# Optimization experiments

Hardware: AMD Instinct MI355X
Metric: run time of the kernel (lower is better)

Reference implementation:

```python
import jax, jax.numpy as jnp
import numpy as np

B, L, E, F, H, V = 64, 32, 512, 512, 1024, 10000


def setup_inputs() -> dict:
    key = jax.random.key(0)
    ks = jax.random.split(key, 20)
    def lin_w(k, out_d, in_d):
        # 4 stacked gate weights (i, f, o, c), PyTorch Linear-style scale
        s = 1.0 / np.sqrt(in_d)
        return jax.random.uniform(k, (4, out_d, in_d), jnp.float32, -s, s)
    def lin_b(k, out_d, in_d):
        s = 1.0 / np.sqrt(in_d)
        return jax.random.uniform(k, (4, out_d), jnp.float32, -s, s)
    inp = {
        "captions": jax.random.randint(ks[0], (B, L), 0, V),
        "image_features": jax.random.normal(ks[1], (B, E), jnp.float32),
        "B_emb": jax.random.normal(ks[2], (V, E), jnp.float32),
        "V_W": lin_w(ks[3], F, E), "V_b": lin_b(ks[4], F, E),
        "S_W": lin_w(ks[5], F, F), "S_b": lin_b(ks[6], F, F),
        "U_W": lin_w(ks[7], H, F), "U_b": lin_b(ks[8], H, F),
        "W_W": lin_w(ks[9], H, H), "W_b": lin_b(ks[10], H, H),
        "C_W": jax.random.uniform(ks[11], (V, H), jnp.float32, -1.0/np.sqrt(H), 1.0/np.sqrt(H)),
        "C_b": jax.random.uniform(ks[12], (V,), jnp.float32, -1.0/np.sqrt(H), 1.0/np.sqrt(H)),
        # original uses nn.init.uniform_ on fresh tensors -> U[0,1)
        "h0": jax.random.uniform(ks[13], (B, H), jnp.float32),
        "c0": jax.random.uniform(ks[14], (B, H), jnp.float32),
    }
    return inp


def reference(captions, image_features, B_emb, V_W, V_b, S_W, S_b, U_W, U_b,
              W_W, W_b, C_W, C_b, h0, c0):
    emb = B_emb[captions]                                   # [B, L, E]
    embedded = jnp.concatenate([image_features[:, None, :], emb], axis=1)  # [B, L+1, E]
    x = embedded[:, :-1, :]                                 # [B, T, E], T = L
    # input-dependent gate pre-activations (V -> S_d[mode] -> U), independent of h
    g = jnp.einsum('bte,gfe->btgf', x, V_W) + V_b           # [B, T, 4, F]
    g = jnp.einsum('btgf,gof->btgo', g, S_W) + S_b          # [B, T, 4, F]
    g = jnp.einsum('btgf,ghf->btgh', g, U_W) + U_b          # [B, T, 4, H]

    def step(carry, g_t):
        h, c = carry
        hg = jnp.einsum('bk,ghk->bgh', h, W_W) + W_b        # [B, 4, H]
        z = g_t + hg
        i_t = jax.nn.sigmoid(z[:, 0])
        f_t = jax.nn.sigmoid(z[:, 1])
        o_t = jax.nn.sigmoid(z[:, 2])
        c_tilda = jnp.tanh(z[:, 3])
        c_new = f_t * c + i_t * c_tilda
        h_new = o_t * c_new
        logits = h_new @ C_W.T + C_b                        # [B, V]
        return (h_new, c_new), logits

    _, outs = jax.lax.scan(step, (h0, c0), jnp.swapaxes(g, 0, 1))  # outs: [T, B, V]
    return jnp.swapaxes(outs, 0, 1)                         # [B, T, V]
```

## Files before the change

### kernel.cpp

```cpp
#include <hip/hip_runtime.h>
#include <hip/hip_bf16.h>

typedef __attribute__((ext_vector_type(8))) __bf16 bf16x8;
typedef __attribute__((ext_vector_type(4))) float f32x4;
typedef unsigned short ushort_t;

#define Bdim 64
#define Tdim 32
#define Edim 512
#define Fdim 512
#define Hdim 1024
#define Vdim 10000
#define SCAN_BLOCKS 64

__device__ __forceinline__ float bf2f(ushort_t u) {
    unsigned int x = ((unsigned int)u) << 16;
    union { unsigned int i; float f; } c; c.i = x; return c.f;
}
__device__ __forceinline__ ushort_t f2bf(float f) {
    __hip_bfloat16 h = __float2bfloat16(f);
    union { __hip_bfloat16 h; ushort_t u; } c; c.h = h; return c.u;
}

__device__ __forceinline__ void gload_lds16(const void* g, void* l) {
    __builtin_amdgcn_global_load_lds(
        (const __attribute__((address_space(1))) unsigned int*)g,
        (__attribute__((address_space(3))) unsigned int*)l, 16, 0, 0);
}

__device__ __forceinline__ void store_short_wt(ushort_t* p, ushort_t v) {
    asm volatile("global_store_short %0, %1, off sc0 sc1"
                 : : "v"(p), "v"((unsigned int)v) : "memory");
}
__device__ __forceinline__ void store_uint_wt(unsigned int* p, unsigned int v) {
    asm volatile("global_store_dword %0, %1, off sc0 sc1"
                 : : "v"(p), "v"(v) : "memory");
}

__global__ void cvt_all(const float* __restrict__ vw, const float* __restrict__ sw,
                        const float* __restrict__ uw, const float* __restrict__ ww,
                        const float* __restrict__ cw, const float* __restrict__ h0,
                        ushort_t* __restrict__ mir, unsigned int* __restrict__ flg) {
    if (blockIdx.x == 0) {
        int4 zz = {0, 0, 0, 0};
        ((int4*)flg)[threadIdx.x * 2 + 0] = zz;
        ((int4*)flg)[threadIdx.x * 2 + 1] = zz;
    }
    long idx = ((long)blockIdx.x * blockDim.x + threadIdx.x) * 8;
    const float* src; long off;
    if      (idx <  1048576L) { src = vw; off = idx; }
    else if (idx <  2097152L) { src = sw; off = idx - 1048576L; }
    else if (idx <  4194304L) { src = uw; off = idx - 2097152L; }
    else if (idx <  8388608L) { src = ww; off = idx - 4194304L; }
    else if (idx < 18628608L) { src = cw; off = idx - 8388608L; }
    else if (idx < 18694144L) { src = h0; off = idx - 18628608L; }
    else return;
    float4 a = *(const float4*)(src + off);
    float4 b = *(const float4*)(src + off + 4);
    ushort_t o[8];
    o[0] = f2bf(a.x); o[1] = f2bf(a.y); o[2] = f2bf(a.z); o[3] = f2bf(a.w);
    o[4] = f2bf(b.x); o[5] = f2bf(b.y); o[6] = f2bf(b.z); o[7] = f2bf(b.w);
    *(int4*)(mir + idx) = *(const int4*)o;
}

__global__ void build_x(const int* __restrict__ cap,
                        const float* __restrict__ img,
                        const float* __restrict__ emb,
                        ushort_t* __restrict__ X) {
    int idx = blockIdx.x * blockDim.x + threadIdx.x;
    int row = idx >> 6;
    int c8  = (idx & 63) << 3;
    int b = row >> 5, t = row & 31;
    const float* src = (t == 0) ? (img + (size_t)b * Edim)
                                : (emb + (size_t)cap[b * Tdim + (t - 1)] * Edim);
    float4 a  = *(const float4*)(src + c8);
    float4 bb = *(const float4*)(src + c8 + 4);
    ushort_t o[8];
    o[0] = f2bf(a.x);  o[1] = f2bf(a.y);  o[2] = f2bf(a.z);  o[3] = f2bf(a.w);
    o[4] = f2bf(bb.x); o[5] = f2bf(bb.y); o[6] = f2bf(bb.z); o[7] = f2bf(bb.w);
    *(int4*)(X + (size_t)row * Edim + c8) = *(const int4*)o;
}

__launch_bounds__(256)
__global__ void gemm_bt(const ushort_t* __restrict__ A, long lda, long gsA,
                        const ushort_t* __restrict__ Bm, long ldb, long gsB,
                        void* __restrict__ Cv, long ldc, long gsC,
                        const float* __restrict__ bias, long gsBias,
                        int N, int K, int f32out, int zpack, int aswap) {
    __shared__ ushort_t As[128 * 64];
    __shared__ ushort_t Bs[128 * 64];
    int z = blockIdx.z;
    A += (size_t)z * gsA; Bm += (size_t)z * gsB; bias += (size_t)z * gsBias;

    int nx = gridDim.x, ny = gridDim.y;
    int lin = blockIdx.x + nx * blockIdx.y;
    int per_xcd = (nx * ny) >> 3;
    int l2 = (lin & 7) * per_xcd + (lin >> 3);
    int bx = l2 / ny, by = l2 % ny;

    int tid = threadIdx.x;
    int w = tid >> 6, l = tid & 63;
    int wm = (w >> 1) * 64, wn = (w & 1) * 64;
    int m0 = by * 128, n0 = bx * 128;

    int srow = tid >> 3;
    int scol = (tid & 7) << 3;

    int lane_r = l & 15;
    int lane_k = (l >> 4) << 3;

    f32x4 zero = {0.f, 0.f, 0.f, 0.f};
    f32x4 acc[4][4];
#pragma unroll
    for (int i = 0; i < 4; i++)
#pragma unroll
        for (int j = 0; j < 4; j++) acc[i][j] = zero;

    for (int k0 = 0; k0 < K; k0 += 64) {
#pragma unroll
        for (int j = 0; j < 4; j++) {
            int r = srow + j * 32;
            int pr = m0 + r;
            if (aswap) pr = ((pr & 31) << 6) + (pr >> 5);
            int sc = scol ^ ((r & 7) << 3);
            gload_lds16(A + (size_t)pr * lda + k0 + sc, &As[r * 64 + scol]);
        }
#pragma unroll
        for (int j = 0; j < 4; j++) {
            int r = srow + j * 32;
            int br = n0 + r; if (br > N - 1) br = N - 1;
            int sc = scol ^ ((r & 7) << 3);
            gload_lds16(Bm + (size_t)br * ldb + k0 + sc, &Bs[r * 64 + scol]);
        }
        __syncthreads();
#pragma unroll
        for (int kk = 0; kk < 64; kk += 32) {
            bf16x8 af[4], bfr[4];
#pragma unroll
            for (int i = 0; i < 4; i++) {
                int ar = wm + i * 16 + lane_r;
                af[i] = *(const bf16x8*)&As[ar * 64 + ((kk + lane_k) ^ ((ar & 7) << 3))];
            }
#pragma unroll
            for (int j = 0; j < 4; j++) {
                int br2 = wn + j * 16 + lane_r;
                bfr[j] = *(const bf16x8*)&Bs[br2 * 64 + ((kk + lane_k) ^ ((br2 & 7) << 3))];
            }
#pragma unroll
            for (int i = 0; i < 4; i++)
#pragma unroll
                for (int j = 0; j < 4; j++)
                    acc[i][j] = __builtin_amdgcn_mfma_f32_16x16x32_bf16(af[i], bfr[j], acc[i][j], 0, 0, 0);
        }
        __syncthreads();
    }

    int row_base = m0 + wm + ((l >> 4) << 2);
    int col_base = n0 + wn + lane_r;
#pragma unroll
    for (int j = 0; j < 4; j++) {
        int col = col_base + j * 16;
        if (col < N) {
            float bv = bias[col];
#pragma unroll
            for (int i = 0; i < 4; i++) {
#pragma unroll
                for (int r = 0; r < 4; r++) {
                    int row = row_base + i * 16 + r;
                    float v = acc[i][j][r] + bv;
                    if (zpack) {
                        int b = row >> 5, tt = row & 31;
                        size_t idx = (((size_t)(tt * 64 + (col >> 4)) * 4 + z) * 16
                                      + (col & 15)) * 64 + b;
                        ((ushort_t*)Cv)[idx] = f2bf(v);
                    } else if (f32out) {
                        ((float*)Cv)[(size_t)z * gsC + (size_t)row * ldc + col] = v;
                    } else {
                        ((ushort_t*)Cv)[(size_t)z * gsC + (size_t)row * ldc + col] = f2bf(v);
                    }
                }
            }
        }
    }
}

#define GLD(i, o) asm volatile("global_load_dwordx4 %0, %1, off offset:" o \
                               : "=v"(ab[i]) : "v"(apx))
#define CHUNK(d, n, ISSUE)                                                                   \
    do {                                                                                     \
        const int kc2 = ((d) * 32 + lane_kb) * 2;                                            \
        bf16x8 b0 = *(const bf16x8*)((const char*)Ws + ((     lane_r) * 2048 + (kc2 ^ swz)));\
        bf16x8 b1 = *(const bf16x8*)((const char*)Ws + ((16 + lane_r) * 2048 + (kc2 ^ swz)));\
        bf16x8 b2 = *(const bf16x8*)((const char*)Ws + ((32 + lane_r) * 2048 + (kc2 ^ swz)));\
        bf16x8 b3 = *(const bf16x8*)((const char*)Ws + ((48 + lane_r) * 2048 + (kc2 ^ swz)));\
        asm volatile("s_waitcnt vmcnt(" n ")");                                              \
        __builtin_amdgcn_sched_barrier(0);                                                   \
        bf16x8 av = __builtin_bit_cast(bf16x8, ab[(d) & 15]);                                \
        acc[0] = __builtin_amdgcn_mfma_f32_16x16x32_bf16(av, b0, acc[0], 0, 0, 0);           \
        acc[1] = __builtin_amdgcn_mfma_f32_16x16x32_bf16(av, b1, acc[1], 0, 0, 0);           \
        acc[2] = __builtin_amdgcn_mfma_f32_16x16x32_bf16(av, b2, acc[2], 0, 0, 0);           \
        acc[3] = __builtin_amdgcn_mfma_f32_16x16x32_bf16(av, b3, acc[3], 0, 0, 0);           \
        ISSUE;                                                                               \
    } while (0)

__launch_bounds__(256, 1)
__global__ void lstm_scan(const ushort_t* __restrict__ Wm,
                          const float* __restrict__ Wb,
                          const ushort_t* __restrict__ zb,
                          const ushort_t* __restrict__ h0b,
                          const float* __restrict__ c0,
                          ushort_t* __restrict__ Hbt,
                          unsigned int* __restrict__ flags) {
    __shared__ ushort_t Ws[64 * 1024];
    int cg = blockIdx.x;
    int tid = threadIdx.x;
    int w = tid >> 6, l = tid & 63;
    int lane_r = l & 15, lane_kb = (l >> 4) << 3;

    for (int e = tid * 8; e < 65536; e += 2048) {
        int rowl = e >> 10, ke = e & 1023;
        int g = rowl >> 4, hc = rowl & 15;
        const ushort_t* src = Wm + ((size_t)(g * Hdim + cg * 16 + hc)) * Hdim + ke;
        int dstb = rowl * 2048 + ((ke * 2) ^ ((rowl & 7) << 4));
        *(int4*)((char*)Ws + dstb) = *(const int4*)src;
    }
    int hcol = cg * 16 + lane_r;
    float wbv[4];
#pragma unroll
    for (int g = 0; g < 4; g++) wbv[g] = Wb[g * Hdim + hcol];
    int rb0 = w * 16 + ((l >> 4) << 2);
    float cst[4];
#pragma unroll
    for (int r = 0; r < 4; r++) cst[r] = c0[(size_t)(rb0 + r) * Hdim + hcol];
    __syncthreads();

    int arow = w * 16 + lane_r;
    int swz = (lane_r & 7) << 4;

    for (int t = 0; t < Tdim; t++) {
        ushort_t g3s[4][4];
        size_t zbase = ((size_t)t * 64 + cg) * 4096 + (size_t)lane_r * 64 + rb0;
#pragma unroll
        for (int g = 0; g < 4; g++)
            *(ushort4*)g3s[g] = *(const ushort4*)(zb + zbase + (size_t)g * 1024);

        if (t > 0) {
            const unsigned int* fp = flags + (size_t)(t - 1) * 64 + l;
            unsigned int v;
            do {
                v = __hip_atomic_load(fp, __ATOMIC_RELAXED, __HIP_MEMORY_SCOPE_AGENT);
            } while (__ballot(v != 0) != 0xFFFFFFFFFFFFFFFFull);
        }
        __builtin_amdgcn_sched_barrier(0);

        const ushort_t* hp = t ? (Hbt + (size_t)(t - 1) * (Bdim * Hdim)) : h0b;
        const ushort_t* apx = hp + (size_t)arow * Hdim + lane_kb;

        int4 ab[16];
        GLD(0, "0");    GLD(1, "64");   GLD(2, "128");  GLD(3, "192");
        GLD(4, "256");  GLD(5, "320");  GLD(6, "384");  GLD(7, "448");
        GLD(8, "512");  GLD(9, "576");  GLD(10, "640"); GLD(11, "704");
        GLD(12, "768"); GLD(13, "832"); GLD(14, "896"); GLD(15, "960");

        f32x4 zero = {0.f, 0.f, 0.f, 0.f};
        f32x4 acc[4];
#pragma unroll
        for (int g = 0; g < 4; g++) acc[g] = zero;

        CHUNK(0, "15", GLD(0, "1024"));  CHUNK(1, "15", GLD(1, "1088"));
        CHUNK(2, "15", GLD(2, "1152"));  CHUNK(3, "15", GLD(3, "1216"));
        CHUNK(4, "15", GLD(4, "1280"));  CHUNK(5, "15", GLD(5, "1344"));
        CHUNK(6, "15", GLD(6, "1408"));  CHUNK(7, "15", GLD(7, "1472"));
        CHUNK(8, "15", GLD(8, "1536"));  CHUNK(9, "15", GLD(9, "1600"));
        CHUNK(10, "15", GLD(10, "1664")); CHUNK(11, "15", GLD(11, "1728"));
        CHUNK(12, "15", GLD(12, "1792")); CHUNK(13, "15", GLD(13, "1856"));
        CHUNK(14, "15", GLD(14, "1920")); CHUNK(15, "15", GLD(15, "1984"));
        CHUNK(16, "15", (void)0); CHUNK(17, "14", (void)0);
        CHUNK(18, "13", (void)0); CHUNK(19, "12", (void)0);
        CHUNK(20, "11", (void)0); CHUNK(21, "10", (void)0);
        CHUNK(22, "9", (void)0);  CHUNK(23, "8", (void)0);
        CHUNK(24, "7", (void)0);  CHUNK(25, "6", (void)0);
        CHUNK(26, "5", (void)0);  CHUNK(27, "4", (void)0);
        CHUNK(28, "3", (void)0);  CHUNK(29, "2", (void)0);
        CHUNK(30, "1", (void)0);  CHUNK(31, "0", (void)0);

#pragma unroll
        for (int r = 0; r < 4; r++) {
            float zi = acc[0][r] + wbv[0] + bf2f(g3s[0][r]);
            float zf = acc[1][r] + wbv[1] + bf2f(g3s[1][r]);
            float zo = acc[2][r] + wbv[2] + bf2f(g3s[2][r]);
            float zc = acc[3][r] + wbv[3] + bf2f(g3s[3][r]);
            float it = __builtin_amdgcn_rcpf(1.f + __expf(-zi));
            float ft = __builtin_amdgcn_rcpf(1.f + __expf(-zf));
            float ot = __builtin_amdgcn_rcpf(1.f + __expf(-zo));
            float e2 = __expf(-2.f * zc);
            float ct = (1.f - e2) * __builtin_amdgcn_rcpf(1.f + e2);
            float cn = ft * cst[r] + it * ct;
            cst[r] = cn;
            store_short_wt(Hbt + (size_t)t * (Bdim * Hdim) + (size_t)(rb0 + r) * Hdim + hcol,
                           f2bf(ot * cn));
        }

        asm volatile("s_waitcnt vmcnt(0)" ::: "memory");
        __syncthreads();
        if (tid == 0) store_uint_wt(flags + (size_t)t * 64 + cg, 1u);
    }
}

extern "C" void kernel_launch(void* const* d_in, const int* in_sizes, int n_in,
                              void* d_out, int out_size, void* d_ws, size_t ws_size,
                              hipStream_t stream) {
    const int*   cap  = (const int*)d_in[0];
    const float* img  = (const float*)d_in[1];
    const float* Bemb = (const float*)d_in[2];
    const float* V_W  = (const float*)d_in[3];
    const float* V_b  = (const float*)d_in[4];
    const float* S_W  = (const float*)d_in[5];
    const float* S_b  = (const float*)d_in[6];
    const float* U_W  = (const float*)d_in[7];
    const float* U_b  = (const float*)d_in[8];
    const float* W_W  = (const float*)d_in[9];
    const float* W_b  = (const float*)d_in[10];
    const float* C_W  = (const float*)d_in[11];
    const float* C_b  = (const float*)d_in[12];
    const float* h0   = (const float*)d_in[13];
    const float* c0   = (const float*)d_in[14];

    char* ws = (char*)d_ws;
    ushort_t* mir = (ushort_t*)(ws);
    ushort_t* X   = (ushort_t*)(ws + (size_t)(36u << 20));
    ushort_t* g1  = (ushort_t*)(ws + (size_t)(38u << 20));
    ushort_t* g2  = (ushort_t*)(ws + (size_t)(46u << 20));
    ushort_t* Hbt = (ushort_t*)(ws + (size_t)(54u << 20));
    unsigned int* flags = (unsigned int*)(ws + (size_t)(58u << 20));
    ushort_t* zb  = (ushort_t*)d_out;

    const ushort_t* V_Wb = mir;
    const ushort_t* S_Wb = mir + 1048576L;
    const ushort_t* U_Wb = mir + 2097152L;
    const ushort_t* W_Wb = mir + 4194304L;
    const ushort_t* C_Wb = mir + 8388608L;
    const ushort_t* h0b  = mir + 18628608L;

    cvt_all<<<9128, 256, 0, stream>>>(V_W, S_W, U_W, W_W, C_W, h0, mir, flags);
    build_x<<<512, 256, 0, stream>>>(cap, img, Bemb, X);

    gemm_bt<<<dim3(16, 16, 1), 256, 0, stream>>>(X, 512, 0, V_Wb, 512, 0,
                                                 g1, 2048, 0, V_b, 0, 2048, 512, 0, 0, 0);
    gemm_bt<<<dim3(4, 16, 4), 256, 0, stream>>>(g1, 2048, 512, S_Wb, 512, 512 * 512,
                                                g2, 2048, 512, S_b, 512, 512, 512, 0, 0, 0);
    gemm_bt<<<dim3(8, 16, 4), 256, 0, stream>>>(g2, 2048, 512, U_Wb, 512, 1024 * 512,
                                                zb, 0, 0, U_b, 1024, 1024, 512, 0, 1, 0);
    {
        const ushort_t* a0 = W_Wb; const float* a1 = W_b; const ushort_t* a2 = zb;
        const ushort_t* a3 = h0b;  const float* a4 = c0;  ushort_t* a5 = Hbt;
        unsigned int* a6 = flags;
        void* sargs[7] = {(void*)&a0, (void*)&a1, (void*)&a2, (void*)&a3,
                          (void*)&a4, (void*)&a5, (void*)&a6};
        hipLaunchCooperativeKernel((const void*)lstm_scan, dim3(SCAN_BLOCKS), dim3(256),
                                   sargs, 0, stream);
    }
    gemm_bt<<<dim3(79, 16, 1), 256, 0, stream>>>(Hbt, 1024, 0, C_Wb, 1024, 0,
                                                 d_out, 10000, 0, C_b, 0,
                                                 10000, 1024, 1, 0, 1);
}
```

Measured before the change: 384.1 us.

## Split LSTM scan across 256 blocks with per-block 4-column gate slices

The recurrent scan now runs on 256 workgroups, each owning 4 hidden columns (16 gate rows) instead of 16 columns, so the per-step W_h matmul work per block drops fourfold and more CUs share the latency-bound loop. Gate pre-activations are packed in a new layout, one MFMA tile covers all four gates, and lane shuffles regroup i/f/o/c per column. Completion flags become bytes polled four at a time as dwords, and the B-operand LDS read is software-pipelined one chunk ahead. The cost is more blocks to synchronise per timestep and redundant h loads across blocks.

Result: slower. 545.4 us (+42.0%).

```diff
diff --git a/kernel.cpp b/kernel.cpp
--- a/kernel.cpp
+++ b/kernel.cpp
@@ -11,7 +11,7 @@
 #define Fdim 512
 #define Hdim 1024
 #define Vdim 10000
-#define SCAN_BLOCKS 64
+#define SCAN_BLOCKS 256
 
 __device__ __forceinline__ float bf2f(ushort_t u) {
     unsigned int x = ((unsigned int)u) << 16;
@@ -32,8 +32,8 @@
     asm volatile("global_store_short %0, %1, off sc0 sc1"
                  : : "v"(p), "v"((unsigned int)v) : "memory");
 }
-__device__ __forceinline__ void store_uint_wt(unsigned int* p, unsigned int v) {
-    asm volatile("global_store_dword %0, %1, off sc0 sc1"
+__device__ __forceinline__ void store_byte_wt(unsigned char* p, unsigned int v) {
+    asm volatile("global_store_byte %0, %1, off sc0 sc1"
                  : : "v"(p), "v"(v) : "memory");
 }
 
@@ -170,8 +170,8 @@
                     float v = acc[i][j][r] + bv;
                     if (zpack) {
                         int b = row >> 5, tt = row & 31;
-                        size_t idx = (((size_t)(tt * 64 + (col >> 4)) * 4 + z) * 16
-                                      + (col & 15)) * 64 + b;
+                        size_t idx = (((size_t)(tt * 256 + (col >> 2)) * 16)
+                                      + (size_t)(z * 4 + (col & 3))) * 64 + b;
                         ((ushort_t*)Cv)[idx] = f2bf(v);
                     } else if (f32out) {
                         ((float*)Cv)[(size_t)z * gsC + (size_t)row * ldc + col] = v;
@@ -188,19 +188,21 @@
                                : "=v"(ab[i]) : "v"(apx))
 #define CHUNK(d, n, ISSUE)                                                                   \
     do {                                                                                     \
-        const int kc2 = ((d) * 32 + lane_kb) * 2;                                            \
-        bf16x8 b0 = *(const bf16x8*)((const char*)Ws + ((     lane_r) * 2048 + (kc2 ^ swz)));\
-        bf16x8 b1 = *(const bf16x8*)((const char*)Ws + ((16 + lane_r) * 2048 + (kc2 ^ swz)));\
-        bf16x8 b2 = *(const bf16x8*)((const char*)Ws + ((32 + lane_r) * 2048 + (kc2 ^ swz)));\
-        bf16x8 b3 = *(const bf16x8*)((const char*)Ws + ((48 + lane_r) * 2048 + (kc2 ^ swz)));\
+        const int kc2n = (((d) + 1) * 32 + lane_kb) * 2;                                     \
+        bf16x8 bnx = *(const bf16x8*)((const char*)Ws + (wrow_b * 2048 + (kc2n ^ swz)));     \
         asm volatile("s_waitcnt vmcnt(" n ")");                                              \
         __builtin_amdgcn_sched_barrier(0);                                                   \
         bf16x8 av = __builtin_bit_cast(bf16x8, ab[(d) & 15]);                                \
-        acc[0] = __builtin_amdgcn_mfma_f32_16x16x32_bf16(av, b0, acc[0], 0, 0, 0);           \
-        acc[1] = __builtin_amdgcn_mfma_f32_16x16x32_bf16(av, b1, acc[1], 0, 0, 0);           \
-        acc[2] = __builtin_amdgcn_mfma_f32_16x16x32_bf16(av, b2, acc[2], 0, 0, 0);           \
-        acc[3] = __builtin_amdgcn_mfma_f32_16x16x32_bf16(av, b3, acc[3], 0, 0, 0);           \
+        acc = __builtin_amdgcn_mfma_f32_16x16x32_bf16(av, bcur, acc, 0, 0, 0);               \
         ISSUE;                                                                               \
+        bcur = bnx;                                                                          \
+    } while (0)
+#define CHUNKL(d, n)                                                                         \
+    do {                                                                                     \
+        asm volatile("s_waitcnt vmcnt(" n ")");                                              \
+        __builtin_amdgcn_sched_barrier(0);                                                   \
+        bf16x8 av = __builtin_bit_cast(bf16x8, ab[(d) & 15]);                                \
+        acc = __builtin_amdgcn_mfma_f32_16x16x32_bf16(av, bcur, acc, 0, 0, 0);               \
     } while (0)
 
 __launch_bounds__(256, 1)
@@ -211,23 +213,21 @@
                           const float* __restrict__ c0,
                           ushort_t* __restrict__ Hbt,
                           unsigned int* __restrict__ flags) {
-    __shared__ ushort_t Ws[64 * 1024];
+    __shared__ ushort_t Ws[16 * 1024];
     int cg = blockIdx.x;
     int tid = threadIdx.x;
     int w = tid >> 6, l = tid & 63;
     int lane_r = l & 15, lane_kb = (l >> 4) << 3;
 
-    for (int e = tid * 8; e < 65536; e += 2048) {
+    for (int e = tid * 8; e < 16384; e += 2048) {
         int rowl = e >> 10, ke = e & 1023;
-        int g = rowl >> 4, hc = rowl & 15;
-        const ushort_t* src = Wm + ((size_t)(g * Hdim + cg * 16 + hc)) * Hdim + ke;
+        const ushort_t* src = Wm + ((size_t)((rowl >> 2) * Hdim + cg * 4 + (rowl & 3))) * Hdim + ke;
         int dstb = rowl * 2048 + ((ke * 2) ^ ((rowl & 7) << 4));
         *(int4*)((char*)Ws + dstb) = *(const int4*)src;
     }
-    int hcol = cg * 16 + lane_r;
-    float wbv[4];
-#pragma unroll
-    for (int g = 0; g < 4; g++) wbv[g] = Wb[g * Hdim + hcol];
+    int hc = l & 3;
+    int hcol = cg * 4 + hc;
+    float wbv = Wb[(lane_r >> 2) * Hdim + hcol - hc + (lane_r & 3)];
     int rb0 = w * 16 + ((l >> 4) << 2);
     float cst[4];
 #pragma unroll
@@ -235,21 +235,18 @@
     __syncthreads();
 
     int arow = w * 16 + lane_r;
-    int swz = (lane_r & 7) << 4;
+    int swz = (l & 7) << 4;
+    int wrow_b = lane_r;
 
     for (int t = 0; t < Tdim; t++) {
-        ushort_t g3s[4][4];
-        size_t zbase = ((size_t)t * 64 + cg) * 4096 + (size_t)lane_r * 64 + rb0;
-#pragma unroll
-        for (int g = 0; g < 4; g++)
-            *(ushort4*)g3s[g] = *(const ushort4*)(zb + zbase + (size_t)g * 1024);
+        ushort4 g3v = *(const ushort4*)(zb + (((size_t)t * 256 + cg) * 16 + lane_r) * 64 + rb0);
 
         if (t > 0) {
             const unsigned int* fp = flags + (size_t)(t - 1) * 64 + l;
             unsigned int v;
             do {
                 v = __hip_atomic_load(fp, __ATOMIC_RELAXED, __HIP_MEMORY_SCOPE_AGENT);
-            } while (__ballot(v != 0) != 0xFFFFFFFFFFFFFFFFull);
+            } while (__ballot(v == 0x01010101u) != 0xFFFFFFFFFFFFFFFFull);
         }
         __builtin_amdgcn_sched_barrier(0);
 
@@ -262,16 +259,14 @@
         GLD(8, "512");  GLD(9, "576");  GLD(10, "640"); GLD(11, "704");
         GLD(12, "768"); GLD(13, "832"); GLD(14, "896"); GLD(15, "960");
 
-        f32x4 zero = {0.f, 0.f, 0.f, 0.f};
-        f32x4 acc[4];
-#pragma unroll
-        for (int g = 0; g < 4; g++) acc[g] = zero;
-
-        CHUNK(0, "15", GLD(0, "1024"));  CHUNK(1, "15", GLD(1, "1088"));
-        CHUNK(2, "15", GLD(2, "1152"));  CHUNK(3, "15", GLD(3, "1216"));
-        CHUNK(4, "15", GLD(4, "1280"));  CHUNK(5, "15", GLD(5, "1344"));
-        CHUNK(6, "15", GLD(6, "1408"));  CHUNK(7, "15", GLD(7, "1472"));
-        CHUNK(8, "15", GLD(8, "1536"));  CHUNK(9, "15", GLD(9, "1600"));
+        f32x4 acc = {0.f, 0.f, 0.f, 0.f};
+        bf16x8 bcur = *(const bf16x8*)((const char*)Ws + (wrow_b * 2048 + ((lane_kb * 2) ^ swz)));
+
+        CHUNK(0, "15", GLD(0, "1024"));   CHUNK(1, "15", GLD(1, "1088"));
+        CHUNK(2, "15", GLD(2, "1152"));   CHUNK(3, "15", GLD(3, "1216"));
+        CHUNK(4, "15", GLD(4, "1280"));   CHUNK(5, "15", GLD(5, "1344"));
+        CHUNK(6, "15", GLD(6, "1408"));   CHUNK(7, "15", GLD(7, "1472"));
+        CHUNK(8, "15", GLD(8, "1536"));   CHUNK(9, "15", GLD(9, "1600"));
         CHUNK(10, "15", GLD(10, "1664")); CHUNK(11, "15", GLD(11, "1728"));
         CHUNK(12, "15", GLD(12, "1792")); CHUNK(13, "15", GLD(13, "1856"));
         CHUNK(14, "15", GLD(14, "1920")); CHUNK(15, "15", GLD(15, "1984"));
@@ -282,14 +277,15 @@
         CHUNK(24, "7", (void)0);  CHUNK(25, "6", (void)0);
         CHUNK(26, "5", (void)0);  CHUNK(27, "4", (void)0);
         CHUNK(28, "3", (void)0);  CHUNK(29, "2", (void)0);
-        CHUNK(30, "1", (void)0);  CHUNK(31, "0", (void)0);
+        CHUNK(30, "1", (void)0);  CHUNKL(31, "0");
 
 #pragma unroll
         for (int r = 0; r < 4; r++) {
-            float zi = acc[0][r] + wbv[0] + bf2f(g3s[0][r]);
-            float zf = acc[1][r] + wbv[1] + bf2f(g3s[1][r]);
-            float zo = acc[2][r] + wbv[2] + bf2f(g3s[2][r]);
-            float zc = acc[3][r] + wbv[3] + bf2f(g3s[3][r]);
+            float zown = acc[r] + wbv + bf2f(g3v[r]);
+            float zi = __shfl(zown, hc,      16);
+            float zf = __shfl(zown, hc + 4,  16);
+            float zo = __shfl(zown, hc + 8,  16);
+            float zc = __shfl(zown, hc + 12, 16);
             float it = __builtin_amdgcn_rcpf(1.f + __expf(-zi));
             float ft = __builtin_amdgcn_rcpf(1.f + __expf(-zf));
             float ot = __builtin_amdgcn_rcpf(1.f + __expf(-zo));
@@ -297,13 +293,14 @@
             float ct = (1.f - e2) * __builtin_amdgcn_rcpf(1.f + e2);
             float cn = ft * cst[r] + it * ct;
             cst[r] = cn;
-            store_short_wt(Hbt + (size_t)t * (Bdim * Hdim) + (size_t)(rb0 + r) * Hdim + hcol,
-                           f2bf(ot * cn));
+            if ((l & 12) == 0)
+                store_short_wt(Hbt + (size_t)t * (Bdim * Hdim) + (size_t)(rb0 + r) * Hdim + hcol,
+                               f2bf(ot * cn));
         }
 
         asm volatile("s_waitcnt vmcnt(0)" ::: "memory");
         __syncthreads();
-        if (tid == 0) store_uint_wt(flags + (size_t)t * 64 + cg, 1u);
+        if (tid == 0) store_byte_wt((unsigned char*)flags + (size_t)t * 256 + cg, 1u);
     }
 }
 
```

## Fuse output projection into LSTM scan via flag-driven consumer blocks

Applied to the files above, without the earlier changes.

Adds 157 consumer blocks to the cooperative scan kernel. Each keeps a 64-row slice of C_W resident in LDS and, as each timestep's h becomes ready (signalled by flags), computes that step's logits and writes them to the output. The aim is to hide the separate vocab-projection GEMM behind the serial recurrence and avoid a kernel launch. In exchange, workspace buffers are relocated, the path only runs when the workspace holds at least 64MB, and the output is written with strided fp32 stores.

Measured after the change: 381.5 us. About the same (-0.7%).

```diff
diff --git a/kernel.cpp b/kernel.cpp
--- a/kernel.cpp
+++ b/kernel.cpp
@@ -12,6 +12,7 @@
 #define Hdim 1024
 #define Vdim 10000
 #define SCAN_BLOCKS 64
+#define CONS_BLOCKS 157
 
 __device__ __forceinline__ float bf2f(ushort_t u) {
     unsigned int x = ((unsigned int)u) << 16;
@@ -202,108 +203,166 @@
         acc[3] = __builtin_amdgcn_mfma_f32_16x16x32_bf16(av, b3, acc[3], 0, 0, 0);           \
         ISSUE;                                                                               \
     } while (0)
+#define KLOOP32()                                                                            \
+    int4 ab[16];                                                                             \
+    GLD(0, "0");    GLD(1, "64");   GLD(2, "128");  GLD(3, "192");                           \
+    GLD(4, "256");  GLD(5, "320");  GLD(6, "384");  GLD(7, "448");                           \
+    GLD(8, "512");  GLD(9, "576");  GLD(10, "640"); GLD(11, "704");                          \
+    GLD(12, "768"); GLD(13, "832"); GLD(14, "896"); GLD(15, "960");                          \
+    CHUNK(0, "15", GLD(0, "1024"));  CHUNK(1, "15", GLD(1, "1088"));                         \
+    CHUNK(2, "15", GLD(2, "1152"));  CHUNK(3, "15", GLD(3, "1216"));                         \
+    CHUNK(4, "15", GLD(4, "1280"));  CHUNK(5, "15", GLD(5, "1344"));                         \
+    CHUNK(6, "15", GLD(6, "1408"));  CHUNK(7, "15", GLD(7, "1472"));                         \
+    CHUNK(8, "15", GLD(8, "1536"));  CHUNK(9, "15", GLD(9, "1600"));                         \
+    CHUNK(10, "15", GLD(10, "1664")); CHUNK(11, "15", GLD(11, "1728"));                      \
+    CHUNK(12, "15", GLD(12, "1792")); CHUNK(13, "15", GLD(13, "1856"));                      \
+    CHUNK(14, "15", GLD(14, "1920")); CHUNK(15, "15", GLD(15, "1984"));                      \
+    CHUNK(16, "15", (void)0); CHUNK(17, "14", (void)0);                                      \
+    CHUNK(18, "13", (void)0); CHUNK(19, "12", (void)0);                                      \
+    CHUNK(20, "11", (void)0); CHUNK(21, "10", (void)0);                                      \
+    CHUNK(22, "9", (void)0);  CHUNK(23, "8", (void)0);                                       \
+    CHUNK(24, "7", (void)0);  CHUNK(25, "6", (void)0);                                       \
+    CHUNK(26, "5", (void)0);  CHUNK(27, "4", (void)0);                                       \
+    CHUNK(28, "3", (void)0);  CHUNK(29, "2", (void)0);                                       \
+    CHUNK(30, "1", (void)0);  CHUNK(31, "0", (void)0)
 
 __launch_bounds__(256, 1)
-__global__ void lstm_scan(const ushort_t* __restrict__ Wm,
-                          const float* __restrict__ Wb,
-                          const ushort_t* __restrict__ zb,
-                          const ushort_t* __restrict__ h0b,
-                          const float* __restrict__ c0,
-                          ushort_t* __restrict__ Hbt,
-                          unsigned int* __restrict__ flags) {
+__global__ void lstm_fused(const ushort_t* __restrict__ Wm,
+                           const float* __restrict__ Wb,
+                           const ushort_t* __restrict__ zb,
+                           const ushort_t* __restrict__ h0b,
+                           const float* __restrict__ c0,
+                           ushort_t* __restrict__ Hbt,
+                           unsigned int* __restrict__ flags,
+                           const ushort_t* __restrict__ CWb,
+                           const float* __restrict__ Cb,
+                           float* __restrict__ out) {
     __shared__ ushort_t Ws[64 * 1024];
-    int cg = blockIdx.x;
+    int bid = blockIdx.x;
     int tid = threadIdx.x;
     int w = tid >> 6, l = tid & 63;
     int lane_r = l & 15, lane_kb = (l >> 4) << 3;
 
-    for (int e = tid * 8; e < 65536; e += 2048) {
-        int rowl = e >> 10, ke = e & 1023;
-        int g = rowl >> 4, hc = rowl & 15;
-        const ushort_t* src = Wm + ((size_t)(g * Hdim + cg * 16 + hc)) * Hdim + ke;
-        int dstb = rowl * 2048 + ((ke * 2) ^ ((rowl & 7) << 4));
-        *(int4*)((char*)Ws + dstb) = *(const int4*)src;
-    }
-    int hcol = cg * 16 + lane_r;
-    float wbv[4];
-#pragma unroll
-    for (int g = 0; g < 4; g++) wbv[g] = Wb[g * Hdim + hcol];
-    int rb0 = w * 16 + ((l >> 4) << 2);
-    float cst[4];
-#pragma unroll
-    for (int r = 0; r < 4; r++) cst[r] = c0[(size_t)(rb0 + r) * Hdim + hcol];
-    __syncthreads();
-
-    int arow = w * 16 + lane_r;
-    int swz = (lane_r & 7) << 4;
-
-    for (int t = 0; t < Tdim; t++) {
-        ushort_t g3s[4][4];
-        size_t zbase = ((size_t)t * 64 + cg) * 4096 + (size_t)lane_r * 64 + rb0;
-#pragma unroll
-        for (int g = 0; g < 4; g++)
-            *(ushort4*)g3s[g] = *(const ushort4*)(zb + zbase + (size_t)g * 1024);
-
-        if (t > 0) {
-            const unsigned int* fp = flags + (size_t)(t - 1) * 64 + l;
-            unsigned int v;
-            do {
-                v = __hip_atomic_load(fp, __ATOMIC_RELAXED, __HIP_MEMORY_SCOPE_AGENT);
-            } while (__ballot(v != 0) != 0xFFFFFFFFFFFFFFFFull);
-        }
-        __builtin_amdgcn_sched_barrier(0);
-
-        const ushort_t* hp = t ? (Hbt + (size_t)(t - 1) * (Bdim * Hdim)) : h0b;
-        const ushort_t* apx = hp + (size_t)arow * Hdim + lane_kb;
-
-        int4 ab[16];
-        GLD(0, "0");    GLD(1, "64");   GLD(2, "128");  GLD(3, "192");
-        GLD(4, "256");  GLD(5, "320");  GLD(6, "384");  GLD(7, "448");
-        GLD(8, "512");  GLD(9, "576");  GLD(10, "640"); GLD(11, "704");
-        GLD(12, "768"); GLD(13, "832"); GLD(14, "896"); GLD(15, "960");
-
-        f32x4 zero = {0.f, 0.f, 0.f, 0.f};
-        f32x4 acc[4];
-#pragma unroll
-        for (int g = 0; g < 4; g++) acc[g] = zero;
-
-        CHUNK(0, "15", GLD(0, "1024"));  CHUNK(1, "15", GLD(1, "1088"));
-        CHUNK(2, "15", GLD(2, "1152"));  CHUNK(3, "15", GLD(3, "1216"));
-        CHUNK(4, "15", GLD(4, "1280"));  CHUNK(5, "15", GLD(5, "1344"));
-        CHUNK(6, "15", GLD(6, "1408"));  CHUNK(7, "15", GLD(7, "1472"));
-        CHUNK(8, "15", GLD(8, "1536"));  CHUNK(9, "15", GLD(9, "1600"));
-        CHUNK(10, "15", GLD(10, "1664")); CHUNK(11, "15", GLD(11, "1728"));
-        CHUNK(12, "15", GLD(12, "1792")); CHUNK(13, "15", GLD(13, "1856"));
-        CHUNK(14, "15", GLD(14, "1920")); CHUNK(15, "15", GLD(15, "1984"));
-        CHUNK(16, "15", (void)0); CHUNK(17, "14", (void)0);
-        CHUNK(18, "13", (void)0); CHUNK(19, "12", (void)0);
-        CHUNK(20, "11", (void)0); CHUNK(21, "10", (void)0);
-        CHUNK(22, "9", (void)0);  CHUNK(23, "8", (void)0);
-        CHUNK(24, "7", (void)0);  CHUNK(25, "6", (void)0);
-        CHUNK(26, "5", (void)0);  CHUNK(27, "4", (void)0);
-        CHUNK(28, "3", (void)0);  CHUNK(29, "2", (void)0);
-        CHUNK(30, "1", (void)0);  CHUNK(31, "0", (void)0);
-
-#pragma unroll
-        for (int r = 0; r < 4; r++) {
-            float zi = acc[0][r] + wbv[0] + bf2f(g3s[0][r]);
-            float zf = acc[1][r] + wbv[1] + bf2f(g3s[1][r]);
-            float zo = acc[2][r] + wbv[2] + bf2f(g3s[2][r]);
-            float zc = acc[3][r] + wbv[3] + bf2f(g3s[3][r]);
-            float it = __builtin_amdgcn_rcpf(1.f + __expf(-zi));
-            float ft = __builtin_amdgcn_rcpf(1.f + __expf(-zf));
-            float ot = __builtin_amdgcn_rcpf(1.f + __expf(-zo));
-            float e2 = __expf(-2.f * zc);
-            float ct = (1.f - e2) * __builtin_amdgcn_rcpf(1.f + e2);
-            float cn = ft * cst[r] + it * ct;
-            cst[r] = cn;
-            store_short_wt(Hbt + (size_t)t * (Bdim * Hdim) + (size_t)(rb0 + r) * Hdim + hcol,
-                           f2bf(ot * cn));
-        }
-
-        asm volatile("s_waitcnt vmcnt(0)" ::: "memory");
+    if (bid < SCAN_BLOCKS) {
+        int cg = bid;
+        for (int e = tid * 8; e < 65536; e += 2048) {
+            int rowl = e >> 10, ke = e & 1023;
+            int g = rowl >> 4, hc = rowl & 15;
+            const ushort_t* src = Wm + ((size_t)(g * Hdim + cg * 16 + hc)) * Hdim + ke;
+            int dstb = rowl * 2048 + ((ke * 2) ^ ((rowl & 7) << 4));
+            *(int4*)((char*)Ws + dstb) = *(const int4*)src;
+        }
+        int hcol = cg * 16 + lane_r;
+        float wbv[4];
+#pragma unroll
+        for (int g = 0; g < 4; g++) wbv[g] = Wb[g * Hdim + hcol];
+        int rb0 = w * 16 + ((l >> 4) << 2);
+        float cst[4];
+#pragma unroll
+        for (int r = 0; r < 4; r++) cst[r] = c0[(size_t)(rb0 + r) * Hdim + hcol];
         __syncthreads();
-        if (tid == 0) store_uint_wt(flags + (size_t)t * 64 + cg, 1u);
+
+        int arow = w * 16 + lane_r;
+        int swz = (lane_r & 7) << 4;
+
+        for (int t = 0; t < Tdim; t++) {
+            ushort_t g3s[4][4];
+            size_t zbase = ((size_t)t * 64 + cg) * 4096 + (size_t)lane_r * 64 + rb0;
+#pragma unroll
+            for (int g = 0; g < 4; g++)
+                *(ushort4*)g3s[g] = *(const ushort4*)(zb + zbase + (size_t)g * 1024);
+
+            if (t > 0) {
+                const unsigned int* fp = flags + (size_t)(t - 1) * 64 + l;
+                unsigned int v;
+                do {
+                    v = __hip_atomic_load(fp, __ATOMIC_RELAXED, __HIP_MEMORY_SCOPE_AGENT);
+                } while (__ballot(v != 0) != 0xFFFFFFFFFFFFFFFFull);
+            }
+            __builtin_amdgcn_sched_barrier(0);
+
+            const ushort_t* hp = t ? (Hbt + (size_t)(t - 1) * (Bdim * Hdim)) : h0b;
+            const ushort_t* apx = hp + (size_t)arow * Hdim + lane_kb;
+
+            f32x4 zero = {0.f, 0.f, 0.f, 0.f};
+            f32x4 acc[4];
+#pragma unroll
+            for (int g = 0; g < 4; g++) acc[g] = zero;
+
+            KLOOP32();
+
+#pragma unroll
+            for (int r = 0; r < 4; r++) {
+                float zi = acc[0][r] + wbv[0] + bf2f(g3s[0][r]);
+                float zf = acc[1][r] + wbv[1] + bf2f(g3s[1][r]);
+                float zo = acc[2][r] + wbv[2] + bf2f(g3s[2][r]);
+                float zc = acc[3][r] + wbv[3] + bf2f(g3s[3][r]);
+                float it = __builtin_amdgcn_rcpf(1.f + __expf(-zi));
+                float ft = __builtin_amdgcn_rcpf(1.f + __expf(-zf));
+                float ot = __builtin_amdgcn_rcpf(1.f + __expf(-zo));
+                float e2 = __expf(-2.f * zc);
+                float ct = (1.f - e2) * __builtin_amdgcn_rcpf(1.f + e2);
+                float cn = ft * cst[r] + it * ct;
+                cst[r] = cn;
+                store_short_wt(Hbt + (size_t)t * (Bdim * Hdim) + (size_t)(rb0 + r) * Hdim + hcol,
+                               f2bf(ot * cn));
+            }
+
+            asm volatile("s_waitcnt vmcnt(0)" ::: "memory");
+            __syncthreads();
+            if (tid == 0) store_uint_wt(flags + (size_t)t * 64 + cg, 1u);
+        }
+    } else {
+        int j = bid - SCAN_BLOCKS;
+        for (int e = tid * 8; e < 65536; e += 2048) {
+            int rowl = e >> 10, ke = e & 1023;
+            int n = j * 64 + rowl; if (n > Vdim - 1) n = Vdim - 1;
+            const ushort_t* src = CWb + (size_t)n * Hdim + ke;
+            int dstb = rowl * 2048 + ((ke * 2) ^ ((rowl & 7) << 4));
+            *(int4*)((char*)Ws + dstb) = *(const int4*)src;
+        }
+        int rb0 = w * 16 + ((l >> 4) << 2);
+        int arow = w * 16 + lane_r;
+        int swz = (lane_r & 7) << 4;
+        float cbv[4];
+#pragma unroll
+        for (int g = 0; g < 4; g++) {
+            int col = j * 64 + g * 16 + lane_r;
+            cbv[g] = Cb[col > Vdim - 1 ? Vdim - 1 : col];
+        }
+        __syncthreads();
+
+        for (int t = 0; t < Tdim; t++) {
+            if (w == 0) {
+                const unsigned int* fp = flags + (size_t)t * 64 + l;
+                unsigned int v;
+                do {
+                    __builtin_amdgcn_s_sleep(8);
+                    v = __hip_atomic_load(fp, __ATOMIC_RELAXED, __HIP_MEMORY_SCOPE_AGENT);
+                } while (__ballot(v != 0) != 0xFFFFFFFFFFFFFFFFull);
+            }
+            __syncthreads();
+            __builtin_amdgcn_sched_barrier(0);
+
+            const ushort_t* apx = Hbt + (size_t)t * (Bdim * Hdim) + (size_t)arow * Hdim + lane_kb;
+
+            f32x4 zero = {0.f, 0.f, 0.f, 0.f};
+            f32x4 acc[4];
+#pragma unroll
+            for (int g = 0; g < 4; g++) acc[g] = zero;
+
+            KLOOP32();
+
+#pragma unroll
+            for (int g = 0; g < 4; g++) {
+                int col = j * 64 + g * 16 + lane_r;
+                if (col < Vdim) {
+#pragma unroll
+                    for (int r = 0; r < 4; r++)
+                        out[((size_t)(rb0 + r) * Tdim + t) * Vdim + col] = acc[g][r] + cbv[g];
+                }
+            }
+        }
     }
 }
 
@@ -327,13 +386,23 @@
     const float* c0   = (const float*)d_in[14];
 
     char* ws = (char*)d_ws;
+    int fused = ws_size >= (size_t)(64u) * 1024 * 1024;
+
     ushort_t* mir = (ushort_t*)(ws);
     ushort_t* X   = (ushort_t*)(ws + (size_t)(36u << 20));
     ushort_t* g1  = (ushort_t*)(ws + (size_t)(38u << 20));
-    ushort_t* g2  = (ushort_t*)(ws + (size_t)(46u << 20));
-    ushort_t* Hbt = (ushort_t*)(ws + (size_t)(54u << 20));
-    unsigned int* flags = (unsigned int*)(ws + (size_t)(58u << 20));
-    ushort_t* zb  = (ushort_t*)d_out;
+    ushort_t *g2, *Hbt, *zbp; unsigned int* flags;
+    if (fused) {
+        zbp   = (ushort_t*)(ws + (size_t)(36u << 20));
+        g2    = (ushort_t*)(ws + (size_t)(52u << 20));
+        Hbt   = (ushort_t*)(ws + (size_t)(60u << 20));
+        flags = (unsigned int*)(ws + (size_t)(36u << 20) - 16384);
+    } else {
+        zbp   = (ushort_t*)d_out;
+        g2    = (ushort_t*)(ws + (size_t)(46u << 20));
+        Hbt   = (ushort_t*)(ws + (size_t)(54u << 20));
+        flags = (unsigned int*)(ws + (size_t)(58u << 20));
+    }
 
     const ushort_t* V_Wb = mir;
     const ushort_t* S_Wb = mir + 1048576L;
@@ -350,17 +419,21 @@
     gemm_bt<<<dim3(4, 16, 4), 256, 0, stream>>>(g1, 2048, 512, S_Wb, 512, 512 * 512,
                                                 g2, 2048, 512, S_b, 512, 512, 512, 0, 0, 0);
     gemm_bt<<<dim3(8, 16, 4), 256, 0, stream>>>(g2, 2048, 512, U_Wb, 512, 1024 * 512,
-                                                zb, 0, 0, U_b, 1024, 1024, 512, 0, 1, 0);
+                                                zbp, 0, 0, U_b, 1024, 1024, 512, 0, 1, 0);
     {
-        const ushort_t* a0 = W_Wb; const float* a1 = W_b; const ushort_t* a2 = zb;
+        const ushort_t* a0 = W_Wb; const float* a1 = W_b; const ushort_t* a2 = zbp;
         const ushort_t* a3 = h0b;  const float* a4 = c0;  ushort_t* a5 = Hbt;
-        unsigned int* a6 = flags;
-        void* sargs[7] = {(void*)&a0, (void*)&a1, (void*)&a2, (void*)&a3,
-                          (void*)&a4, (void*)&a5, (void*)&a6};
-        hipLaunchCooperativeKernel((const void*)lstm_scan, dim3(SCAN_BLOCKS), dim3(256),
+        unsigned int* a6 = flags;  const ushort_t* a7 = C_Wb; const float* a8 = C_b;
+        float* a9 = (float*)d_out;
+        void* sargs[10] = {(void*)&a0, (void*)&a1, (void*)&a2, (void*)&a3, (void*)&a4,
+                           (void*)&a5, (void*)&a6, (void*)&a7, (void*)&a8, (void*)&a9};
+        int grid = fused ? (SCAN_BLOCKS + CONS_BLOCKS) : SCAN_BLOCKS;
+        hipLaunchCooperativeKernel((const void*)lstm_fused, dim3(grid), dim3(256),
                                    sargs, 0, stream);
     }
-    gemm_bt<<<dim3(79, 16, 1), 256, 0, stream>>>(Hbt, 1024, 0, C_Wb, 1024, 0,
-                                                 d_out, 10000, 0, C_b, 0,
-                                                 10000, 1024, 1, 0, 1);
-}
+    if (!fused) {
+        gemm_bt<<<dim3(79, 16, 1), 256, 0, stream>>>(Hbt, 1024, 0, C_Wb, 1024, 0,
+                                                     d_out, 10000, 0, C_b, 0,
+                                                     10000, 1024, 1, 0, 1);
+    }
+}
```
